# Optimization experiments

Measured on AMD Instinct MI355X. Metric: run time of the kernel, lower is better.

## Reference

```python
import jax, jax.numpy as jnp
import numpy as np

B, S = 64, 4096
IN_CH, HID, OUT_CH, LIFT, MODES, NLAYERS = 2, 64, 3, 256, 16, 4
FREQ = S // 2 + 1


def setup_inputs() -> dict:
    key = jax.random.key(0)
    ks = jax.random.split(key, 10)
    g = lambda k, shp, s=0.02: (jax.random.normal(k, shp, jnp.float32) * s)
    return {
        "x": jax.random.normal(ks[0], (B, S, IN_CH), jnp.float32),
        "lift_w1": g(ks[1], (LIFT, IN_CH), 0.1),
        "lift_b1": jnp.zeros((LIFT,), jnp.float32),
        "lift_w2": g(ks[2], (HID, LIFT)),
        "lift_b2": jnp.zeros((HID,), jnp.float32),
        # spectral weights per layer: real/imag parts of [in, out, modes]
        "spec_wr": g(ks[3], (NLAYERS, HID, HID, MODES), 1.0 / HID),
        "spec_wi": g(ks[4], (NLAYERS, HID, HID, MODES), 1.0 / HID),
        "skip_w": g(ks[5], (NLAYERS, HID, HID)),
        "skip_b": jnp.zeros((NLAYERS, HID), jnp.float32),
        "proj_w1": g(ks[6], (LIFT, HID)),
        "proj_b1": jnp.zeros((LIFT,), jnp.float32),
        "proj_w2": g(ks[7], (OUT_CH, LIFT)),
        "proj_b2": jnp.zeros((OUT_CH,), jnp.float32),
    }


def _gelu(x):
    return jax.nn.gelu(x, approximate=False)  # torch F.gelu default (exact)


def reference(x, lift_w1, lift_b1, lift_w2, lift_b2, spec_wr, spec_wi,
              skip_w, skip_b, proj_w1, proj_b1, proj_w2, proj_b2):
    # x: (B, S, 2) -> permute to channels-first (B, 2, S), fused into einsum
    h = jnp.einsum('bsi,oi->bos', x, lift_w1) + lift_b1[None, :, None]  # (B, 256, S)
    h = _gelu(h)
    h = jnp.einsum('bcs,oc->bos', h, lift_w2) + lift_b2[None, :, None]  # (B, 64, S)

    for l in range(NLAYERS):
        # spectral conv: rfft -> keep low modes -> complex mix -> irfft
        xf = jnp.fft.rfft(h, axis=-1)[..., :MODES]            # (B, HID, MODES) complex
        w = spec_wr[l] + 1j * spec_wi[l]                       # (HID, HID, MODES)
        yk = jnp.einsum('bim,iom->bom', xf, w)                 # (B, HID, MODES)
        yf = jnp.zeros((h.shape[0], HID, FREQ), jnp.complex64).at[..., :MODES].set(yk)
        spec = jnp.fft.irfft(yf, n=S, axis=-1)                 # (B, HID, S)
        skip = jnp.einsum('bcs,oc->bos', h, skip_w[l]) + skip_b[l][None, :, None]
        h = spec + skip
        if l < NLAYERS - 1:
            h = _gelu(h)

    h = _gelu(jnp.einsum('bcs,oc->bos', h, proj_w1) + proj_b1[None, :, None])
    out_seq = jnp.einsum('bcs,oc->bos', h, proj_w2) + proj_b2[None, :, None]  # (B, 3, S)
    # AdaptiveAvgPool1d(1) + squeeze(-1) == mean over length
    return out_seq.mean(axis=-1)  # (B, 3)
```

## Files before the change

kernel.cpp:

```cpp
#include <hip/hip_runtime.h>
#include <math.h>

#define B_    64
#define S_    4096
#define HID   64
#define LIFT  256
#define MODES 16
#define NL    4

#define OFF_H     0
#define OFF_ETB   16777216
#define OFF_XFY   (OFF_ETB + 131072)
#define OFF_SKH   (OFF_XFY + 131072)
#define OFF_SKL   (OFF_SKH + 8192)
#define OFF_W2HI  (OFF_SKL + 8192)
#define OFF_W2LO  (OFF_W2HI + 8192)
#define OFF_P1HI  (OFF_W2LO + 8192)
#define OFF_P1LO  (OFF_P1HI + 8192)
#define OFF_PART  (OFF_P1LO + 8192)
#define OFF_W1B   (OFF_PART + 12288)

typedef short short8 __attribute__((ext_vector_type(8)));
typedef float f32x4  __attribute__((ext_vector_type(4)));
typedef unsigned uint8v __attribute__((ext_vector_type(8)));
#define MFMA16 __builtin_amdgcn_mfma_f32_16x16x32_bf16

__device__ __forceinline__ float gelu_f(float x) {
  return 0.5f * x * (1.0f + erff(x * 0.70710678118654752440f));
}
__device__ __forceinline__ unsigned short f2bf(float x) {
  unsigned u = __float_as_uint(x);
  u += 0x7fffu + ((u >> 16) & 1u);
  return (unsigned short)(u >> 16);
}
__device__ __forceinline__ float bf2f(unsigned short b) {
  return __uint_as_float(((unsigned)b) << 16);
}
__device__ __forceinline__ unsigned packsplit(float x) {
  unsigned short hi = f2bf(x);
  unsigned short lo = f2bf(x - bf2f(hi));
  return (unsigned)hi | ((unsigned)lo << 16);
}
__device__ __forceinline__ void unpk8(const unsigned* pk, short8& h8, short8& l8) {
  #pragma unroll
  for (int j = 0; j < 8; ++j) {
    unsigned u = pk[j];
    h8[j] = (short)(u & 0xffffu);
    l8[j] = (short)(u >> 16);
  }
}

__global__ void k_init(const float* __restrict__ lift_w2,
                       const float* __restrict__ skip_w,
                       const float* __restrict__ proj_w1,
                       const float* __restrict__ lift_w1,
                       const float* __restrict__ lift_b1,
                       float* __restrict__ ws) {
  unsigned* etab = (unsigned*)(ws + OFF_ETB);
  unsigned short* skh = (unsigned short*)(ws + OFF_SKH);
  unsigned short* skl = (unsigned short*)(ws + OFF_SKL);
  unsigned short* w2hi = (unsigned short*)(ws + OFF_W2HI);
  unsigned short* w2lo = (unsigned short*)(ws + OFF_W2LO);
  unsigned short* p1hi = (unsigned short*)(ws + OFF_P1HI);
  unsigned short* p1lo = (unsigned short*)(ws + OFF_P1LO);
  float4* w1b = (float4*)(ws + OFF_W1B);
  int idx = blockIdx.x * 256 + threadIdx.x;
  int stride = gridDim.x * 256;
  for (int k = idx; k < 4096 * 32; k += stride) {
    int s = k >> 5, c = k & 31;
    int m = c & 15;
    int r = (m * s) & 4095;
    float th = (float)(2.0 * 3.14159265358979323846 / 4096.0) * (float)r;
    float sn, cn; sincosf(th, &sn, &cn);
    float v = (c < 16) ? cn : -sn;
    etab[k] = packsplit(v);
  }
  for (int k = idx; k < NL * HID * HID; k += stride) {
    float w = skip_w[k];
    unsigned short hi = f2bf(w);
    skh[k] = hi; skl[k] = f2bf(w - bf2f(hi));
  }
  for (int k = idx; k < HID * LIFT; k += stride) {
    float w = lift_w2[k];
    unsigned short hi = f2bf(w);
    w2hi[k] = hi; w2lo[k] = f2bf(w - bf2f(hi));
  }
  for (int k = idx; k < LIFT * HID; k += stride) {
    float w = proj_w1[k];
    unsigned short hi = f2bf(w);
    p1hi[k] = hi; p1lo[k] = f2bf(w - bf2f(hi));
  }
  for (int k = idx; k < LIFT; k += stride) {
    w1b[k] = make_float4(lift_w1[2 * k], lift_w1[2 * k + 1], lift_b1[k], 0.f);
  }
  for (int k = idx; k < 12288; k += stride)
    ws[OFF_PART + k] = 0.f;
}

__global__ __launch_bounds__(256, 2) void k_lift(
    const float* __restrict__ x, const float4* __restrict__ W1B,
    const float* __restrict__ b2,
    const unsigned short* __restrict__ Whi,
    const unsigned short* __restrict__ Wlo,
    unsigned* __restrict__ Hp) {
  int tid = threadIdx.x;
  int b = blockIdx.y, s0 = blockIdx.x * 256;
  int lane = tid & 63, wv = tid >> 6, quad = lane >> 4, n16 = lane & 15;
  int sw = s0 + wv * 64;
  int cq = quad * 8;
  float2 xv[4];
  #pragma unroll
  for (int nt = 0; nt < 4; ++nt)
    xv[nt] = ((const float2*)x)[b * S_ + sw + nt * 16 + n16];
  f32x4 acc[4][4];
  #pragma unroll
  for (int mt = 0; mt < 4; ++mt)
    #pragma unroll
    for (int nt = 0; nt < 4; ++nt) acc[mt][nt] = (f32x4){0.f, 0.f, 0.f, 0.f};

  #pragma unroll 1
  for (int k = 0; k < 8; ++k) {
    short8 ah[4], al[4];
    #pragma unroll
    for (int mt = 0; mt < 4; ++mt) {
      int aoff = (mt * 16 + n16) * 256 + k * 32 + cq;
      ah[mt] = *(const short8*)(Whi + aoff);
      al[mt] = *(const short8*)(Wlo + aoff);
    }
    float4 w[8];
    #pragma unroll
    for (int j = 0; j < 8; ++j) w[j] = W1B[k * 32 + cq + j];
    #pragma unroll
    for (int nt = 0; nt < 4; ++nt) {
      short8 bh, bl;
      #pragma unroll
      for (int j = 0; j < 8; ++j) {
        float t = gelu_f(w[j].x * xv[nt].x + w[j].y * xv[nt].y + w[j].z);
        unsigned pk = packsplit(t);
        bh[j] = (short)(pk & 0xffffu);
        bl[j] = (short)(pk >> 16);
      }
      #pragma unroll
      for (int mt = 0; mt < 4; ++mt) {
        acc[mt][nt] = MFMA16(ah[mt], bh, acc[mt][nt], 0, 0, 0);
        acc[mt][nt] = MFMA16(ah[mt], bl, acc[mt][nt], 0, 0, 0);
        acc[mt][nt] = MFMA16(al[mt], bh, acc[mt][nt], 0, 0, 0);
      }
    }
  }
  #pragma unroll
  for (int mt = 0; mt < 4; ++mt) {
    int o0 = mt * 16 + quad * 4;
    float4 bb = *(const float4*)&b2[o0];
    #pragma unroll
    for (int nt = 0; nt < 4; ++nt) {
      int sc = sw + nt * 16 + n16;
      unsigned* hp = Hp + ((size_t)b * HID + o0) * S_ + sc;
      hp[0]            = packsplit(acc[mt][nt][0] + bb.x);
      hp[(size_t)S_]   = packsplit(acc[mt][nt][1] + bb.y);
      hp[(size_t)2*S_] = packsplit(acc[mt][nt][2] + bb.z);
      hp[(size_t)3*S_] = packsplit(acc[mt][nt][3] + bb.w);
    }
  }
}

__global__ __launch_bounds__(256, 4) void k_fft_fwd(
    const unsigned* __restrict__ Hp, const unsigned* __restrict__ Etab,
    float* __restrict__ xf) {
  __shared__ float red[4 * 512];
  int tid = threadIdx.x;
  int i0 = blockIdx.x * 16, b = blockIdx.y, ks = blockIdx.z;
  int lane = tid & 63, wv = tid >> 6, quad = lane >> 4, n16 = lane & 15;
  const unsigned* hb = Hp + ((size_t)b * HID + i0 + n16) * S_;
  int g = ks * 4 + wv;
  f32x4 acc0 = (f32x4){0.f,0.f,0.f,0.f}, acc1 = (f32x4){0.f,0.f,0.f,0.f};
  #pragma unroll 1
  for (int kt = 0; kt < 8; ++kt) {
    int sb = g * 256 + kt * 32 + quad * 8;
    uint8v av = *(const uint8v*)(hb + sb);
    short8 ah, al;
    #pragma unroll
    for (int j = 0; j < 8; ++j) {
      unsigned u = av[j];
      ah[j] = (short)(u & 0xffffu); al[j] = (short)(u >> 16);
    }
    unsigned q0[8], q1[8];
    #pragma unroll
    for (int j = 0; j < 8; ++j) {
      q0[j] = Etab[(sb + j) * 32 + n16];
      q1[j] = Etab[(sb + j) * 32 + 16 + n16];
    }
    short8 bh0, bl0, bh1, bl1;
    unpk8(q0, bh0, bl0);
    unpk8(q1, bh1, bl1);
    acc0 = MFMA16(ah, bh0, acc0, 0, 0, 0);
    acc0 = MFMA16(ah, bl0, acc0, 0, 0, 0);
    acc0 = MFMA16(al, bh0, acc0, 0, 0, 0);
    acc1 = MFMA16(ah, bh1, acc1, 0, 0, 0);
    acc1 = MFMA16(ah, bl1, acc1, 0, 0, 0);
    acc1 = MFMA16(al, bh1, acc1, 0, 0, 0);
  }
  #pragma unroll
  for (int r = 0; r < 4; ++r) {
    red[wv * 512 + (quad * 4 + r) * 32 + n16]      = acc0[r];
    red[wv * 512 + (quad * 4 + r) * 32 + 16 + n16] = acc1[r];
  }
  __syncthreads();
  #pragma unroll
  for (int u = 0; u < 2; ++u) {
    int t = u * 256 + tid;
    int il = t >> 5, c = t & 31;
    float v = red[t] + red[512 + t] + red[1024 + t] + red[1536 + t];
    atomicAdd(&xf[(size_t)b * 2048 + (i0 + il) * 32 + c], v);
  }
}

__global__ __launch_bounds__(256) void k_mix(
    const float* __restrict__ wr_, const float* __restrict__ wi_,
    float* __restrict__ xfy) {
  int tid = threadIdx.x;
  int b = blockIdx.x;
  __shared__ float xr[HID * MODES], xi[HID * MODES];
  const float* xfb = xfy + (size_t)b * 2048;
  for (int u = tid; u < HID * MODES; u += 256) {
    int i = u >> 4, m = u & 15;
    xr[u] = xfb[i * 32 + m];
    xi[u] = xfb[i * 32 + 16 + m];
  }
  __syncthreads();
  const float invS = 1.0f / (float)S_;
  unsigned* yk = (unsigned*)xfy + (size_t)b * 2048;
  #pragma unroll
  for (int pp = 0; pp < 4; ++pp) {
    int p = pp * 256 + tid;
    int o = p >> 4, m = p & 15;
    float yr = 0.f, yi = 0.f;
    for (int i2 = 0; i2 < HID; ++i2) {
      float wr = wr_[(i2 * HID + o) * MODES + m];
      float wi = wi_[(i2 * HID + o) * MODES + m];
      float xrv = xr[i2 * MODES + m], xiv = xi[i2 * MODES + m];
      yr += xrv * wr - xiv * wi;
      yi += xrv * wi + xiv * wr;
    }
    float fac = (m == 0) ? invS : 2.f * invS;
    yk[o * 32 + m]      = packsplit(yr * fac);
    yk[o * 32 + 16 + m] = packsplit(yi * fac);
  }
}

template <bool ACT>
__global__ __launch_bounds__(256, 2) void k_spec_skip(
    const unsigned short* __restrict__ Shi,
    const unsigned short* __restrict__ Slo,
    const float* __restrict__ skb,
    const unsigned* __restrict__ Yk,
    const unsigned* __restrict__ Etab,
    unsigned* __restrict__ Hp) {
  int tid = threadIdx.x;
  int s0 = blockIdx.x * 256, b = blockIdx.y;
  int lane = tid & 63, wv = tid >> 6, quad = lane >> 4, n16 = lane & 15;
  int sw = s0 + wv * 64;
  f32x4 acc[4][4];
  #pragma unroll
  for (int mt = 0; mt < 4; ++mt)
    #pragma unroll
    for (int nt = 0; nt < 4; ++nt) acc[mt][nt] = (f32x4){0.f,0.f,0.f,0.f};
  {
    short8 yh[4], yl[4];
    #pragma unroll
    for (int mt = 0; mt < 4; ++mt) {
      uint8v yv = *(const uint8v*)(Yk + (size_t)b * 2048 + (mt * 16 + n16) * 32 + quad * 8);
      #pragma unroll
      for (int j = 0; j < 8; ++j) {
        unsigned u = yv[j];
        yh[mt][j] = (short)(u & 0xffffu); yl[mt][j] = (short)(u >> 16);
      }
    }
    #pragma unroll
    for (int nt = 0; nt < 4; ++nt) {
      int sc = sw + nt * 16 + n16;
      uint8v tv = *(const uint8v*)(Etab + (size_t)sc * 32 + quad * 8);
      short8 th, tl;
      #pragma unroll
      for (int j = 0; j < 8; ++j) {
        unsigned u = tv[j];
        th[j] = (short)(u & 0xffffu); tl[j] = (short)(u >> 16);
      }
      #pragma unroll
      for (int mt = 0; mt < 4; ++mt) {
        acc[mt][nt] = MFMA16(yh[mt], th, acc[mt][nt], 0, 0, 0);
        acc[mt][nt] = MFMA16(yh[mt], tl, acc[mt][nt], 0, 0, 0);
        acc[mt][nt] = MFMA16(yl[mt], th, acc[mt][nt], 0, 0, 0);
      }
    }
  }
  const unsigned* hb = Hp + (size_t)b * HID * S_;
  #pragma unroll
  for (int kk = 0; kk < 2; ++kk) {
    short8 skh[4], skl[4];
    #pragma unroll
    for (int mt = 0; mt < 4; ++mt) {
      int off = (mt * 16 + n16) * 64 + kk * 32 + quad * 8;
      skh[mt] = *(const short8*)(Shi + off);
      skl[mt] = *(const short8*)(Slo + off);
    }
    #pragma unroll
    for (int nt = 0; nt < 4; ++nt) {
      int sc = sw + nt * 16 + n16;
      unsigned pk[8];
      #pragma unroll
      for (int j = 0; j < 8; ++j)
        pk[j] = hb[(size_t)(kk * 32 + quad * 8 + j) * S_ + sc];
      short8 bh, bl;
      unpk8(pk, bh, bl);
      #pragma unroll
      for (int mt = 0; mt < 4; ++mt) {
        acc[mt][nt] = MFMA16(skh[mt], bh, acc[mt][nt], 0, 0, 0);
        acc[mt][nt] = MFMA16(skh[mt], bl, acc[mt][nt], 0, 0, 0);
        acc[mt][nt] = MFMA16(skl[mt], bh, acc[mt][nt], 0, 0, 0);
      }
    }
  }
  #pragma unroll
  for (int mt = 0; mt < 4; ++mt) {
    int o0 = mt * 16 + quad * 4;
    float4 bb = *(const float4*)&skb[o0];
    #pragma unroll
    for (int nt = 0; nt < 4; ++nt) {
      int sc = sw + nt * 16 + n16;
      #pragma unroll
      for (int r = 0; r < 4; ++r) {
        float v = acc[mt][nt][r] + ((const float*)&bb)[r];
        if (ACT) v = gelu_f(v);
        Hp[(size_t)(b * HID + o0 + r) * S_ + sc] = packsplit(v);
      }
    }
  }
}

__global__ __launch_bounds__(256, 2) void k_proj(
    const unsigned short* __restrict__ Phi,
    const unsigned short* __restrict__ Plo,
    const float* __restrict__ pb1, const float* __restrict__ pw2,
    const unsigned* __restrict__ Hp, float* __restrict__ part) {
  __shared__ unsigned Bp[64 * 65];
  __shared__ float red[12];
  int tid = threadIdx.x;
  int s0 = blockIdx.x * 64, b = blockIdx.y;
  int lane = tid & 63, wv = tid >> 6, quad = lane >> 4, n16 = lane & 15;
  #pragma unroll
  for (int u = 0; u < 16; ++u) {
    int idx = u * 256 + tid;
    int c = idx >> 6, s = idx & 63;
    Bp[c * 65 + s] = Hp[((size_t)b * HID + c) * S_ + s0 + s];
  }
  __syncthreads();
  int m0 = blockIdx.z * 128 + wv * 32;
  f32x4 acc[2][4];
  #pragma unroll
  for (int mt = 0; mt < 2; ++mt)
    #pragma unroll
    for (int nt = 0; nt < 4; ++nt) acc[mt][nt] = (f32x4){0.f,0.f,0.f,0.f};
  #pragma unroll
  for (int kk = 0; kk < 2; ++kk) {
    int kbase = kk * 32 + quad * 8;
    short8 ah[2], al[2];
    #pragma unroll
    for (int mt = 0; mt < 2; ++mt) {
      int aoff = (m0 + mt * 16 + n16) * 64 + kbase;
      ah[mt] = *(const short8*)(Phi + aoff);
      al[mt] = *(const short8*)(Plo + aoff);
    }
    #pragma unroll
    for (int nt = 0; nt < 4; ++nt) {
      int sc = nt * 16 + n16;
      unsigned pk[8];
      #pragma unroll
      for (int j = 0; j < 8; ++j) pk[j] = Bp[(kbase + j) * 65 + sc];
      short8 bh, bl;
      unpk8(pk, bh, bl);
      #pragma unroll
      for (int mt = 0; mt < 2; ++mt) {
        acc[mt][nt] = MFMA16(ah[mt], bh, acc[mt][nt], 0, 0, 0);
        acc[mt][nt] = MFMA16(ah[mt], bl, acc[mt][nt], 0, 0, 0);
        acc[mt][nt] = MFMA16(al[mt], bh, acc[mt][nt], 0, 0, 0);
      }
    }
  }
  float o0 = 0.f, o1 = 0.f, o2 = 0.f;
  #pragma unroll
  for (int mt = 0; mt < 2; ++mt) {
    int c2b = m0 + mt * 16 + quad * 4;
    float4 bb = *(const float4*)&pb1[c2b];
    float4 p0 = *(const float4*)&pw2[c2b];
    float4 p1 = *(const float4*)&pw2[256 + c2b];
    float4 p2 = *(const float4*)&pw2[512 + c2b];
    #pragma unroll
    for (int nt = 0; nt < 4; ++nt) {
      f32x4 a = acc[mt][nt];
      float t0 = gelu_f(a[0] + bb.x);
      float t1 = gelu_f(a[1] + bb.y);
      float t2 = gelu_f(a[2] + bb.z);
      float t3 = gelu_f(a[3] + bb.w);
      o0 += p0.x * t0 + p0.y * t1 + p0.z * t2 + p0.w * t3;
      o1 += p1.x * t0 + p1.y * t1 + p1.z * t2 + p1.w * t3;
      o2 += p2.x * t0 + p2.y * t1 + p2.z * t2 + p2.w * t3;
    }
  }
  #pragma unroll
  for (int off = 32; off > 0; off >>= 1) {
    o0 += __shfl_xor(o0, off, 64);
    o1 += __shfl_xor(o1, off, 64);
    o2 += __shfl_xor(o2, off, 64);
  }
  if (lane == 0) { red[wv*3+0] = o0; red[wv*3+1] = o1; red[wv*3+2] = o2; }
  __syncthreads();
  if (tid < 3) {
    float sum = red[tid] + red[3 + tid] + red[6 + tid] + red[9 + tid];
    atomicAdd(&part[(b * 64 + blockIdx.x) * 3 + tid], sum);
  }
}

__global__ void k_final(const float* __restrict__ part,
                        const float* __restrict__ pb2,
                        float* __restrict__ out) {
  int t = threadIdx.x;
  if (t < B_ * 3) {
    int b = t / 3, j = t % 3;
    float s = 0.f;
    for (int k = 0; k < 64; ++k) s += part[(b * 64 + k) * 3 + j];
    out[t] = s * (1.0f / (float)S_) + pb2[j];
  }
}

extern "C" void kernel_launch(void* const* d_in, const int* in_sizes, int n_in,
                              void* d_out, int out_size, void* d_ws, size_t ws_size,
                              hipStream_t stream) {
  const float* x   = (const float*)d_in[0];
  const float* lw1 = (const float*)d_in[1];
  const float* lb1 = (const float*)d_in[2];
  const float* lw2 = (const float*)d_in[3];
  const float* lb2 = (const float*)d_in[4];
  const float* swr = (const float*)d_in[5];
  const float* swi = (const float*)d_in[6];
  const float* skw = (const float*)d_in[7];
  const float* skb = (const float*)d_in[8];
  const float* pw1 = (const float*)d_in[9];
  const float* pb1 = (const float*)d_in[10];
  const float* pw2 = (const float*)d_in[11];
  const float* pb2 = (const float*)d_in[12];
  float* ws = (float*)d_ws;
  unsigned* Hp  = (unsigned*)(ws + OFF_H);
  unsigned* ETB = (unsigned*)(ws + OFF_ETB);
  float*    XFY = ws + OFF_XFY;

  k_init<<<256, 256, 0, stream>>>(lw2, skw, pw1, lw1, lb1, ws);
  k_lift<<<dim3(S_ / 256, B_), 256, 0, stream>>>(
      x, (const float4*)(ws + OFF_W1B), lb2,
      (const unsigned short*)(ws + OFF_W2HI),
      (const unsigned short*)(ws + OFF_W2LO), Hp);
  for (int l = 0; l < NL; ++l) {
    hipMemsetAsync(XFY, 0, (size_t)B_ * 2048 * sizeof(float), stream);
    k_fft_fwd<<<dim3(4, B_, 4), 256, 0, stream>>>(Hp, ETB, XFY);
    k_mix<<<B_, 256, 0, stream>>>(swr + l * HID * HID * MODES,
                                  swi + l * HID * HID * MODES, XFY);
    if (l < NL - 1)
      k_spec_skip<true><<<dim3(S_ / 256, B_), 256, 0, stream>>>(
          (const unsigned short*)(ws + OFF_SKH) + l * HID * HID,
          (const unsigned short*)(ws + OFF_SKL) + l * HID * HID,
          skb + l * HID, (const unsigned*)XFY, ETB, Hp);
    else
      k_spec_skip<false><<<dim3(S_ / 256, B_), 256, 0, stream>>>(
          (const unsigned short*)(ws + OFF_SKH) + l * HID * HID,
          (const unsigned short*)(ws + OFF_SKL) + l * HID * HID,
          skb + l * HID, (const unsigned*)XFY, ETB, Hp);
  }
  k_proj<<<dim3(S_ / 64, B_, 2), 256, 0, stream>>>(
      (const unsigned short*)(ws + OFF_P1HI),
      (const unsigned short*)(ws + OFF_P1LO),
      pb1, pw2, Hp, ws + OFF_PART);
  k_final<<<1, 256, 0, stream>>>(ws + OFF_PART, pb2, (float*)d_out);
}
```

Baseline: 547.0 us.

## Switch hidden activation buffer from channel-major to sequence-major layout

The packed hi/lo bf16 hidden-state buffer is stored as [B][S][HID] instead of [B][HID][S]. The lift and layer epilogues can then write four consecutive channels with one 16-byte store, and the skip-path B-operand load becomes a single 32-byte vector load instead of eight strided loads. The forward-FFT A-operand load now becomes eight strided loads at stride HID, and the projection staging reads channel-contiguous data.

After: 588.6 us. +7.6%, slower.

```diff
diff --git a/kernel.cpp b/kernel.cpp
--- a/kernel.cpp
+++ b/kernel.cpp
@@ -23,6 +23,7 @@
 typedef short short8 __attribute__((ext_vector_type(8)));
 typedef float f32x4  __attribute__((ext_vector_type(4)));
 typedef unsigned uint8v __attribute__((ext_vector_type(8)));
+typedef unsigned uint4v __attribute__((ext_vector_type(4)));
 #define MFMA16 __builtin_amdgcn_mfma_f32_16x16x32_bf16
 
 __device__ __forceinline__ float gelu_f(float x) {
@@ -155,11 +156,12 @@
     #pragma unroll
     for (int nt = 0; nt < 4; ++nt) {
       int sc = sw + nt * 16 + n16;
-      unsigned* hp = Hp + ((size_t)b * HID + o0) * S_ + sc;
-      hp[0]            = packsplit(acc[mt][nt][0] + bb.x);
-      hp[(size_t)S_]   = packsplit(acc[mt][nt][1] + bb.y);
-      hp[(size_t)2*S_] = packsplit(acc[mt][nt][2] + bb.z);
-      hp[(size_t)3*S_] = packsplit(acc[mt][nt][3] + bb.w);
+      uint4v v;
+      v[0] = packsplit(acc[mt][nt][0] + bb.x);
+      v[1] = packsplit(acc[mt][nt][1] + bb.y);
+      v[2] = packsplit(acc[mt][nt][2] + bb.z);
+      v[3] = packsplit(acc[mt][nt][3] + bb.w);
+      *(uint4v*)&Hp[((size_t)b * S_ + sc) * HID + o0] = v;
     }
   }
 }
@@ -171,19 +173,18 @@
   int tid = threadIdx.x;
   int i0 = blockIdx.x * 16, b = blockIdx.y, ks = blockIdx.z;
   int lane = tid & 63, wv = tid >> 6, quad = lane >> 4, n16 = lane & 15;
-  const unsigned* hb = Hp + ((size_t)b * HID + i0 + n16) * S_;
+  const unsigned* hb = Hp + (size_t)b * S_ * HID + i0 + n16;
   int g = ks * 4 + wv;
   f32x4 acc0 = (f32x4){0.f,0.f,0.f,0.f}, acc1 = (f32x4){0.f,0.f,0.f,0.f};
   #pragma unroll 1
   for (int kt = 0; kt < 8; ++kt) {
     int sb = g * 256 + kt * 32 + quad * 8;
-    uint8v av = *(const uint8v*)(hb + sb);
+    unsigned aU[8];
+    #pragma unroll
+    for (int j = 0; j < 8; ++j)
+      aU[j] = hb[(size_t)(sb + j) * HID];
     short8 ah, al;
-    #pragma unroll
-    for (int j = 0; j < 8; ++j) {
-      unsigned u = av[j];
-      ah[j] = (short)(u & 0xffffu); al[j] = (short)(u >> 16);
-    }
+    unpk8(aU, ah, al);
     unsigned q0[8], q1[8];
     #pragma unroll
     for (int j = 0; j < 8; ++j) {
@@ -294,7 +295,7 @@
       }
     }
   }
-  const unsigned* hb = Hp + (size_t)b * HID * S_;
+  const unsigned* hb = Hp + (size_t)b * S_ * HID;
   #pragma unroll
   for (int kk = 0; kk < 2; ++kk) {
     short8 skh[4], skl[4];
@@ -307,12 +308,13 @@
     #pragma unroll
     for (int nt = 0; nt < 4; ++nt) {
       int sc = sw + nt * 16 + n16;
-      unsigned pk[8];
-      #pragma unroll
-      for (int j = 0; j < 8; ++j)
-        pk[j] = hb[(size_t)(kk * 32 + quad * 8 + j) * S_ + sc];
+      uint8v hv = *(const uint8v*)(hb + (size_t)sc * HID + kk * 32 + quad * 8);
       short8 bh, bl;
-      unpk8(pk, bh, bl);
+      #pragma unroll
+      for (int j = 0; j < 8; ++j) {
+        unsigned u = hv[j];
+        bh[j] = (short)(u & 0xffffu); bl[j] = (short)(u >> 16);
+      }
       #pragma unroll
       for (int mt = 0; mt < 4; ++mt) {
         acc[mt][nt] = MFMA16(skh[mt], bh, acc[mt][nt], 0, 0, 0);
@@ -328,12 +330,14 @@
     #pragma unroll
     for (int nt = 0; nt < 4; ++nt) {
       int sc = sw + nt * 16 + n16;
+      uint4v v;
       #pragma unroll
       for (int r = 0; r < 4; ++r) {
-        float v = acc[mt][nt][r] + ((const float*)&bb)[r];
-        if (ACT) v = gelu_f(v);
-        Hp[(size_t)(b * HID + o0 + r) * S_ + sc] = packsplit(v);
-      }
+        float val = acc[mt][nt][r] + ((const float*)&bb)[r];
+        if (ACT) val = gelu_f(val);
+        v[r] = packsplit(val);
+      }
+      *(uint4v*)&Hp[((size_t)b * S_ + sc) * HID + o0] = v;
     }
   }
 }
@@ -351,8 +355,8 @@
   #pragma unroll
   for (int u = 0; u < 16; ++u) {
     int idx = u * 256 + tid;
-    int c = idx >> 6, s = idx & 63;
-    Bp[c * 65 + s] = Hp[((size_t)b * HID + c) * S_ + s0 + s];
+    int s = idx >> 6, c = idx & 63;
+    Bp[c * 65 + s] = Hp[((size_t)b * S_ + s0 + s) * HID + c];
   }
   __syncthreads();
   int m0 = blockIdx.z * 128 + wv * 32;
```
